# Performance work log

Hardware: AMD Instinct MI355X
Metric: run time of the kernel (lower is better)

Reference implementation:

```python
import jax, jax.numpy as jnp
import numpy as np

BETA = 0.25
GAMMA = 0.9
EPS = 1e-05
B, H, W, D, K = 64, 32, 32, 256, 1024


def setup_inputs() -> dict:
    key = jax.random.key(0)
    k1, k2 = jax.random.split(key)
    return {
        "inputs": jax.random.normal(k1, (B, H, W, D), dtype=jnp.float32),
        "codebook": jax.random.normal(k2, (D, K), dtype=jnp.float32),
        "ema_hidden_cluster": jnp.zeros((K,), dtype=jnp.float32),
        "ema_hidden_dw": jnp.zeros((D, K), dtype=jnp.float32),
        "counter": 1,  # counter after increment (fresh state: 0 + 1)
    }


def reference(inputs, codebook, ema_hidden_cluster, ema_hidden_dw, counter):
    d, k = codebook.shape
    flat = inputs.reshape(-1, d)  # [N, D]
    distances = (
        jnp.sum(jnp.square(flat), 1, keepdims=True)
        - 2.0 * jnp.matmul(flat, codebook)
        + jnp.sum(jnp.square(codebook), 0, keepdims=True)
    )
    encoding_indices = jnp.argmin(distances, axis=1)  # [N]
    encodings = jax.nn.one_hot(encoding_indices, k, dtype=distances.dtype)  # [N, K]
    flat_quantized = jnp.take(codebook, encoding_indices, axis=1).swapaxes(1, 0)  # [N, D]
    quantized = flat_quantized.reshape(inputs.shape)
    loss = BETA * jnp.mean(jnp.square(jax.lax.stop_gradient(quantized) - inputs))

    # --- EMA codebook update (training=True path) ---
    decay = jnp.float32(GAMMA)
    one = jnp.float32(1.0)
    bias = one - jnp.power(decay, counter)
    cluster_size = jnp.sum(encodings, axis=0)  # [K]
    hid_cs = ema_hidden_cluster * decay + cluster_size * (one - decay)
    avg_cs = hid_cs / bias
    dw = jnp.matmul(flat.T, encodings)  # [D, K]
    hid_dw = ema_hidden_dw * decay + dw * (one - decay)
    avg_dw = hid_dw / bias
    n = jnp.sum(avg_cs)
    smoothed_cs = (avg_cs + EPS) / (n + k * EPS) * n
    new_codebook = avg_dw / smoothed_cs[None, :]

    ste = inputs + jax.lax.stop_gradient(quantized - inputs)
    avg_probs = jnp.mean(encodings, 0)
    perplexity = jnp.exp(-jnp.sum(avg_probs * jnp.log(avg_probs + 1e-10)))
    return (ste, perplexity, loss, new_codebook)
```

## Files before the change

kernel.cpp:

```cpp
#include <hip/hip_runtime.h>

#define N 65536
#define D 256
#define K 1024
#define BETA 0.25f
#define GAMMA 0.9f
#define EPS 1e-5f

#define DWROWS 64

#define OFF_INDICES 0
#define OFF_PERM    262144
#define OFF_COUNTS  524288
#define OFF_CNORM   528384
#define OFF_OFFSETS 532480
#define OFF_CURSOR  536576
#define OFF_SMOOTH  540672
#define OFF_LOSSP   544768
#define OFF_CBT     546816
#define OFF_CBE     1595392

typedef __bf16 bf16x8 __attribute__((ext_vector_type(8)));
typedef short  s16x8  __attribute__((ext_vector_type(8)));
typedef float  f32x4  __attribute__((ext_vector_type(4)));

__device__ inline unsigned short f32_to_bf16_rn(float f) {
    unsigned int u = __float_as_uint(f);
    unsigned int r = u + 0x7fffu + ((u >> 16) & 1u);
    return (unsigned short)(r >> 16);
}

__device__ inline f32x4 mfma16(s16x8 a, s16x8 b, f32x4 c) {
    return __builtin_amdgcn_mfma_f32_16x16x32_bf16(
        __builtin_bit_cast(bf16x8, a), __builtin_bit_cast(bf16x8, b), c, 0, 0, 0);
}

__device__ __forceinline__ void stage16(const s16x8* __restrict__ g, s16x8* l) {
    __builtin_amdgcn_global_load_lds(
        (const __attribute__((address_space(1))) void*)g,
        (__attribute__((address_space(3))) void*)l, 16, 0, 0);
}

__global__ __launch_bounds__(256) void pack_cb(const float* __restrict__ cb,
                                               float* __restrict__ cbT,
                                               s16x8* __restrict__ cbEp,
                                               float* __restrict__ cnorm) {
    const int ct = blockIdx.x >> 2;
    const int c2 = blockIdx.x & 3;
#pragma unroll
    for (int it = 0; it < 2; ++it) {
        int u = it * 256 + threadIdx.x;
        int frgc = u >> 7;
        int ks = (u >> 6) & 1;
        int L = u & 63;
        int c = ct * 64 + frgc * 16 + (L & 15);
        int d0 = c2 * 64 + (ks * 4 + (L >> 4)) * 8;
        float v[8];
        s16x8 hv, lv;
        float ss = 0.f;
#pragma unroll
        for (int j = 0; j < 8; ++j) {
            float f = cb[(size_t)(d0 + j) * K + c];
            v[j] = f;
            unsigned short h = f32_to_bf16_rn(f);
            hv[j] = (short)h;
            lv[j] = (short)f32_to_bf16_rn(f - __uint_as_float((unsigned)h << 16));
            ss = fmaf(f, f, ss);
        }
        *(float4*)&cbT[(size_t)c * D + d0]     = make_float4(v[0], v[1], v[2], v[3]);
        *(float4*)&cbT[(size_t)c * D + d0 + 4] = make_float4(v[4], v[5], v[6], v[7]);
        cbEp[(size_t)(ct * 8 + c2) * 512 + u]     = hv;
        cbEp[(size_t)(ct * 8 + 4 + c2) * 512 + u] = lv;
        atomicAdd(&cnorm[c], ss);
    }
}

__global__ __launch_bounds__(256, 2) void argmin_mfma_kernel(
        const float* __restrict__ x,
        const s16x8* __restrict__ cbEp,
        const float* __restrict__ cnorm,
        int* __restrict__ indices) {
    __shared__ s16x8 Bs[2][1024];

    const int tid = threadIdx.x;
    const int lane = tid & 63;
    const int w = tid >> 6;
    const int r0 = blockIdx.x * 128;
    const int row16 = lane & 15;
    const int quad = lane >> 4;

#pragma unroll
    for (int i = 0; i < 4; ++i)
        stage16(cbEp + i * 256 + tid, &Bs[0][i * 256 + w * 64]);

    s16x8 Ah[2][8], Al[2][8];
#pragma unroll
    for (int frg = 0; frg < 2; ++frg) {
#pragma unroll
        for (int kb8 = 0; kb8 < 8; ++kb8) {
            const float* src = &x[(size_t)(r0 + w * 32 + frg * 16 + row16) * D
                                  + kb8 * 32 + quad * 8];
            float4 v0 = *(const float4*)src;
            float4 v1 = *(const float4*)(src + 4);
            float f[8] = {v0.x, v0.y, v0.z, v0.w, v1.x, v1.y, v1.z, v1.w};
            s16x8 hv, lv;
#pragma unroll
            for (int j = 0; j < 8; ++j) {
                unsigned short h = f32_to_bf16_rn(f[j]);
                hv[j] = (short)h;
                lv[j] = (short)f32_to_bf16_rn(f[j] - __uint_as_float((unsigned)h << 16));
            }
            Ah[frg][kb8] = hv;
            Al[frg][kb8] = lv;
        }
    }

    float minv[2][4];
    int   mini[2][4];
#pragma unroll
    for (int frg = 0; frg < 2; ++frg)
#pragma unroll
        for (int reg = 0; reg < 4; ++reg) { minv[frg][reg] = 3.4e38f; mini[frg][reg] = 0; }

    for (int ct = 0; ct < 16; ++ct) {
        f32x4 acc[2][4];
#pragma unroll
        for (int frg = 0; frg < 2; ++frg)
#pragma unroll
            for (int fc = 0; fc < 4; ++fc) acc[frg][fc] = (f32x4){0.f, 0.f, 0.f, 0.f};

#pragma unroll
        for (int ph = 0; ph < 4; ++ph) {
            __syncthreads();
            const bool has_next = !(ct == 15 && ph == 3);
            if (has_next) {
                const int nct = (ph == 3) ? ct + 1 : ct;
                const int nph = (ph == 3) ? 0 : ph + 1;
                const size_t gb = (size_t)(nct * 8 + nph * 2) * 512;
#pragma unroll
                for (int i = 0; i < 4; ++i)
                    stage16(cbEp + gb + i * 256 + tid, &Bs[(ph + 1) & 1][i * 256 + w * 64]);
            }
#pragma unroll
            for (int half = 0; half < 2; ++half) {
                const int cchunk = ph * 2 + half;
                const int c2 = cchunk & 3;
#pragma unroll
                for (int ks = 0; ks < 2; ++ks) {
                    const int ksb = c2 * 2 + ks;
#pragma unroll
                    for (int fc = 0; fc < 4; ++fc) {
                        s16x8 b = Bs[ph & 1][half * 512 + (fc * 2 + ks) * 64 + lane];
#pragma unroll
                        for (int frg = 0; frg < 2; ++frg) {
                            acc[frg][fc] = mfma16(Ah[frg][ksb], b, acc[frg][fc]);
                            if (cchunk < 4)
                                acc[frg][fc] = mfma16(Al[frg][ksb], b, acc[frg][fc]);
                        }
                    }
                }
            }
        }
#pragma unroll
        for (int fc = 0; fc < 4; ++fc) {
            int col = ct * 64 + fc * 16 + row16;
            float cn = cnorm[col];
#pragma unroll
            for (int frg = 0; frg < 2; ++frg)
#pragma unroll
                for (int reg = 0; reg < 4; ++reg) {
                    float val = fmaf(-2.f, acc[frg][fc][reg], cn);
                    if (val < minv[frg][reg]) { minv[frg][reg] = val; mini[frg][reg] = col; }
                }
        }
    }

#pragma unroll
    for (int mask = 1; mask <= 8; mask <<= 1) {
#pragma unroll
        for (int frg = 0; frg < 2; ++frg)
#pragma unroll
            for (int reg = 0; reg < 4; ++reg) {
                float ov = __shfl_xor(minv[frg][reg], mask, 64);
                int   oi = __shfl_xor(mini[frg][reg], mask, 64);
                if (ov < minv[frg][reg] ||
                    (ov == minv[frg][reg] && oi < mini[frg][reg])) {
                    minv[frg][reg] = ov; mini[frg][reg] = oi;
                }
            }
    }
    if (row16 == 0) {
#pragma unroll
        for (int frg = 0; frg < 2; ++frg)
#pragma unroll
            for (int reg = 0; reg < 4; ++reg)
                indices[r0 + w * 32 + frg * 16 + quad * 4 + reg] = mini[frg][reg];
    }
}

__global__ __launch_bounds__(1024) void finalize_kernel(const int* __restrict__ indices,
                                                        const float* __restrict__ ema_c,
                                                        const int* __restrict__ counter,
                                                        float* __restrict__ out_perp,
                                                        int* __restrict__ cursor,
                                                        float* __restrict__ smoothed) {
    const int k = threadIdx.x;
    __shared__ int hist[1024];
    __shared__ float fred[1024];
    __shared__ int scan[1024];
    __shared__ float nsum_s;

    hist[k] = 0;
    __syncthreads();
    const int4* idx4 = (const int4*)indices;
#pragma unroll 4
    for (int i = 0; i < 16; ++i) {
        int4 v = idx4[(size_t)i * 1024 + k];
        atomicAdd(&hist[v.x], 1);
        atomicAdd(&hist[v.y], 1);
        atomicAdd(&hist[v.z], 1);
        atomicAdd(&hist[v.w], 1);
    }
    __syncthreads();

    const int c = hist[k];
    const float bias = 1.0f - powf(GAMMA, (float)counter[0]);
    const float hid = fmaf(ema_c[k], GAMMA, (float)c * (1.0f - GAMMA));
    const float avg = hid / bias;

    fred[k] = avg;
    __syncthreads();
    for (int s = 512; s >= 1; s >>= 1) {
        if (k < s) fred[k] += fred[k + s];
        __syncthreads();
    }
    if (k == 0) nsum_s = fred[0];
    __syncthreads();
    const float nsum = nsum_s;

    float p = (float)c * (1.0f / (float)N);
    fred[k] = p * logf(p + 1e-10f);
    __syncthreads();
    for (int s = 512; s >= 1; s >>= 1) {
        if (k < s) fred[k] += fred[k + s];
        __syncthreads();
    }
    if (k == 0) out_perp[0] = expf(-fred[0]);

    scan[k] = c;
    __syncthreads();
    for (int s = 1; s < 1024; s <<= 1) {
        int v = (k >= s) ? scan[k - s] : 0;
        __syncthreads();
        scan[k] += v;
        __syncthreads();
    }
    cursor[k] = scan[k] - c;

    smoothed[k] = (avg + EPS) / (nsum + (float)K * EPS) * nsum;
}

__global__ __launch_bounds__(256) void scatter_kernel(const int* __restrict__ indices,
                                                      int* __restrict__ cursor,
                                                      int* __restrict__ permk,
                                                      float* __restrict__ dwT) {
    const int n = blockIdx.x * 256 + threadIdx.x;
    *(float4*)&dwT[(size_t)n * 4] = make_float4(0.f, 0.f, 0.f, 0.f);
    const int k = indices[n];
    const int pos = atomicAdd(&cursor[k], 1);
    permk[pos] = n | (k << 16);
}

__global__ __launch_bounds__(256) void dw_fused_kernel(const float* __restrict__ x,
                                                       const float* __restrict__ cbT,
                                                       const int* __restrict__ permk,
                                                       float* __restrict__ ste,
                                                       float* __restrict__ dwT,
                                                       float* __restrict__ lossp) {
    __shared__ int s_rows[DWROWS];
    __shared__ int s_keys[DWROWS + 1];
    const int d = threadIdx.x;
    const int base = blockIdx.x * DWROWS;
    if (threadIdx.x < DWROWS) {
        const int pk = permk[base + threadIdx.x];
        s_rows[threadIdx.x] = pk & 0xffff;
        s_keys[threadIdx.x] = pk >> 16;
    }
    if (threadIdx.x == 0) s_keys[DWROWS] = -1;
    __syncthreads();
    float acc = 0.f;
    float ls = 0.f;
#pragma unroll 4
    for (int i = 0; i < DWROWS; ++i) {
        const int n = s_rows[i];
        const int k = s_keys[i];
        const float xv = x[(size_t)n * D + d];
        const float q  = cbT[(size_t)k * D + d];
        ste[(size_t)n * D + d] = q;
        acc += xv;
        const float df = q - xv;
        ls = fmaf(df, df, ls);
        if (s_keys[i + 1] != k) {
            atomicAdd(&dwT[(size_t)k * D + d], acc);
            acc = 0.f;
        }
    }
#pragma unroll
    for (int off = 32; off >= 1; off >>= 1) ls += __shfl_down(ls, off, 64);
    __shared__ float red[4];
    if ((d & 63) == 0) red[d >> 6] = ls;
    __syncthreads();
    if (d == 0) lossp[blockIdx.x] = red[0] + red[1] + red[2] + red[3];
}

__global__ __launch_bounds__(256) void codebook_final_kernel(const float* __restrict__ dwT,
                                                             const float* __restrict__ ema_dw,
                                                             const float* __restrict__ smoothed,
                                                             const int* __restrict__ counter,
                                                             const float* __restrict__ lossp,
                                                             float* __restrict__ out_cb,
                                                             float* __restrict__ out_loss) {
    __shared__ float tile[64][65];
    __shared__ float lred[4];
    const int tid = threadIdx.x;

    if (blockIdx.x == 0) {
        float s = lossp[tid] + lossp[tid + 256] + lossp[tid + 512] + lossp[tid + 768];
#pragma unroll
        for (int off = 32; off >= 1; off >>= 1) s += __shfl_down(s, off, 64);
        if ((tid & 63) == 0) lred[tid >> 6] = s;
        __syncthreads();
        if (tid == 0)
            out_loss[0] = BETA * (lred[0] + lred[1] + lred[2] + lred[3])
                          * (1.0f / ((float)N * (float)D));
        __syncthreads();
    }

    const int d0 = (blockIdx.x & 3) * 64;
    const int k0 = (blockIdx.x >> 2) * 64;
#pragma unroll
    for (int it = 0; it < 16; ++it) {
        int idx = it * 256 + tid;
        int kk = idx >> 6, dd = idx & 63;
        tile[kk][dd] = dwT[(size_t)(k0 + kk) * D + d0 + dd];
    }
    __syncthreads();
    const float bias = 1.0f - powf(GAMMA, (float)counter[0]);
#pragma unroll
    for (int it = 0; it < 16; ++it) {
        int idx = it * 256 + tid;
        int dd = idx >> 6, kk = idx & 63;
        float dwv = tile[kk][dd];
        float hid = fmaf(ema_dw[(size_t)(d0 + dd) * K + k0 + kk], GAMMA,
                         dwv * (1.0f - GAMMA));
        out_cb[(size_t)(d0 + dd) * K + k0 + kk] = (hid / bias) / smoothed[k0 + kk];
    }
}

extern "C" void kernel_launch(void* const* d_in, const int* in_sizes, int n_in,
                              void* d_out, int out_size, void* d_ws, size_t ws_size,
                              hipStream_t stream) {
    const float* x       = (const float*)d_in[0];
    const float* cb      = (const float*)d_in[1];
    const float* ema_c   = (const float*)d_in[2];
    const float* ema_dw  = (const float*)d_in[3];
    const int*   counter = (const int*)d_in[4];

    float* out = (float*)d_out;
    float* ste = out;
    float* out_perp = out + (size_t)N * D;
    float* out_loss = out_perp + 1;
    float* out_cb = out_perp + 2;

    char* ws = (char*)d_ws;
    int* indices  = (int*)(ws + OFF_INDICES);
    int* permk    = (int*)(ws + OFF_PERM);
    float* cnorm  = (float*)(ws + OFF_CNORM);
    int* cursor   = (int*)(ws + OFF_CURSOR);
    float* smooth = (float*)(ws + OFF_SMOOTH);
    float* cbT    = (float*)(ws + OFF_CBT);
    s16x8* cbEp   = (s16x8*)(ws + OFF_CBE);
    float* dwT    = (float*)(ws + OFF_CBE);
    float* lossp  = (float*)(ws + OFF_CNORM);

    hipMemsetAsync(cnorm, 0, K * sizeof(float), stream);

    pack_cb<<<64, 256, 0, stream>>>(cb, cbT, cbEp, cnorm);
    argmin_mfma_kernel<<<N / 128, 256, 0, stream>>>(x, cbEp, cnorm, indices);
    finalize_kernel<<<1, 1024, 0, stream>>>(indices, ema_c, counter,
                                            out_perp, cursor, smooth);
    scatter_kernel<<<N / 256, 256, 0, stream>>>(indices, cursor, permk, dwT);
    dw_fused_kernel<<<N / DWROWS, 256, 0, stream>>>(x, cbT, permk, ste, dwT, lossp);
    codebook_final_kernel<<<64, 256, 0, stream>>>(dwT, ema_dw, smooth, counter,
                                                  lossp, out_cb, out_loss);
}
```

Baseline: 287.2 us.

## Vectorize dw gather, use wave shuffles in finalize, double pack_cb grid

Three separate changes. pack_cb now runs one item per thread across twice as many blocks. finalize_kernel replaces its shared-memory tree reductions and Hillis-Steele scan, with their many block barriers, by wave-level shuffle reductions and scans plus one barrier. dw_fused_kernel switches to float4 loads and stores, with each wave handling 16 rows, which cuts the load count but splits segment flushes per wave and adds four atomics per flush.

After: 308.6 us. 7.5% more time.

```diff
diff --git a/kernel.cpp b/kernel.cpp
--- a/kernel.cpp
+++ b/kernel.cpp
@@ -45,34 +45,32 @@
                                                float* __restrict__ cbT,
                                                s16x8* __restrict__ cbEp,
                                                float* __restrict__ cnorm) {
-    const int ct = blockIdx.x >> 2;
-    const int c2 = blockIdx.x & 3;
-#pragma unroll
-    for (int it = 0; it < 2; ++it) {
-        int u = it * 256 + threadIdx.x;
-        int frgc = u >> 7;
-        int ks = (u >> 6) & 1;
-        int L = u & 63;
-        int c = ct * 64 + frgc * 16 + (L & 15);
-        int d0 = c2 * 64 + (ks * 4 + (L >> 4)) * 8;
-        float v[8];
-        s16x8 hv, lv;
-        float ss = 0.f;
-#pragma unroll
-        for (int j = 0; j < 8; ++j) {
-            float f = cb[(size_t)(d0 + j) * K + c];
-            v[j] = f;
-            unsigned short h = f32_to_bf16_rn(f);
-            hv[j] = (short)h;
-            lv[j] = (short)f32_to_bf16_rn(f - __uint_as_float((unsigned)h << 16));
-            ss = fmaf(f, f, ss);
-        }
-        *(float4*)&cbT[(size_t)c * D + d0]     = make_float4(v[0], v[1], v[2], v[3]);
-        *(float4*)&cbT[(size_t)c * D + d0 + 4] = make_float4(v[4], v[5], v[6], v[7]);
-        cbEp[(size_t)(ct * 8 + c2) * 512 + u]     = hv;
-        cbEp[(size_t)(ct * 8 + 4 + c2) * 512 + u] = lv;
-        atomicAdd(&cnorm[c], ss);
-    }
+    const int ct = blockIdx.x >> 3;
+    const int c2 = (blockIdx.x >> 1) & 3;
+    const int half = blockIdx.x & 1;
+    const int u = half * 256 + threadIdx.x;
+    const int frgc = u >> 7;
+    const int ks = (u >> 6) & 1;
+    const int L = u & 63;
+    const int c = ct * 64 + frgc * 16 + (L & 15);
+    const int d0 = c2 * 64 + (ks * 4 + (L >> 4)) * 8;
+    float v[8];
+    s16x8 hv, lv;
+    float ss = 0.f;
+#pragma unroll
+    for (int j = 0; j < 8; ++j) {
+        float f = cb[(size_t)(d0 + j) * K + c];
+        v[j] = f;
+        unsigned short h = f32_to_bf16_rn(f);
+        hv[j] = (short)h;
+        lv[j] = (short)f32_to_bf16_rn(f - __uint_as_float((unsigned)h << 16));
+        ss = fmaf(f, f, ss);
+    }
+    *(float4*)&cbT[(size_t)c * D + d0]     = make_float4(v[0], v[1], v[2], v[3]);
+    *(float4*)&cbT[(size_t)c * D + d0 + 4] = make_float4(v[4], v[5], v[6], v[7]);
+    cbEp[(size_t)(ct * 8 + c2) * 512 + u]     = hv;
+    cbEp[(size_t)(ct * 8 + 4 + c2) * 512 + u] = lv;
+    atomicAdd(&cnorm[c], ss);
 }
 
 __global__ __launch_bounds__(256, 2) void argmin_mfma_kernel(
@@ -205,10 +203,11 @@
                                                         int* __restrict__ cursor,
                                                         float* __restrict__ smoothed) {
     const int k = threadIdx.x;
+    const int lane = k & 63;
+    const int wave = k >> 6;
     __shared__ int hist[1024];
-    __shared__ float fred[1024];
-    __shared__ int scan[1024];
-    __shared__ float nsum_s;
+    __shared__ float wsum[16], went[16];
+    __shared__ int wtot[16];
 
     hist[k] = 0;
     __syncthreads();
@@ -225,39 +224,37 @@
 
     const int c = hist[k];
     const float bias = 1.0f - powf(GAMMA, (float)counter[0]);
-    const float hid = fmaf(ema_c[k], GAMMA, (float)c * (1.0f - GAMMA));
-    const float avg = hid / bias;
-
-    fred[k] = avg;
-    __syncthreads();
-    for (int s = 512; s >= 1; s >>= 1) {
-        if (k < s) fred[k] += fred[k + s];
-        __syncthreads();
-    }
-    if (k == 0) nsum_s = fred[0];
-    __syncthreads();
-    const float nsum = nsum_s;
-
-    float p = (float)c * (1.0f / (float)N);
-    fred[k] = p * logf(p + 1e-10f);
-    __syncthreads();
-    for (int s = 512; s >= 1; s >>= 1) {
-        if (k < s) fred[k] += fred[k + s];
-        __syncthreads();
-    }
-    if (k == 0) out_perp[0] = expf(-fred[0]);
-
-    scan[k] = c;
-    __syncthreads();
-    for (int s = 1; s < 1024; s <<= 1) {
-        int v = (k >= s) ? scan[k - s] : 0;
-        __syncthreads();
-        scan[k] += v;
-        __syncthreads();
-    }
-    cursor[k] = scan[k] - c;
-
+    const float avg = fmaf(ema_c[k], GAMMA, (float)c * (1.0f - GAMMA)) / bias;
+    const float p = (float)c * (1.0f / (float)N);
+    const float ent = p * logf(p + 1e-10f);
+
+    float a = avg, e = ent;
+#pragma unroll
+    for (int off = 32; off >= 1; off >>= 1) {
+        a += __shfl_down(a, off, 64);
+        e += __shfl_down(e, off, 64);
+    }
+    int v = c;
+#pragma unroll
+    for (int off = 1; off < 64; off <<= 1) {
+        int t = __shfl_up(v, off, 64);
+        if (lane >= off) v += t;
+    }
+    if (lane == 0)  { wsum[wave] = a; went[wave] = e; }
+    if (lane == 63) { wtot[wave] = v; }
+    __syncthreads();
+
+    float nsum = 0.f, entt = 0.f;
+    int woff = 0;
+#pragma unroll
+    for (int i = 0; i < 16; ++i) {
+        nsum += wsum[i];
+        entt += went[i];
+        if (i < wave) woff += wtot[i];
+    }
+    cursor[k] = woff + v - c;
     smoothed[k] = (avg + EPS) / (nsum + (float)K * EPS) * nsum;
+    if (k == 0) out_perp[0] = expf(-entt);
 }
 
 __global__ __launch_bounds__(256) void scatter_kernel(const int* __restrict__ indices,
@@ -278,39 +275,53 @@
                                                        float* __restrict__ dwT,
                                                        float* __restrict__ lossp) {
     __shared__ int s_rows[DWROWS];
-    __shared__ int s_keys[DWROWS + 1];
-    const int d = threadIdx.x;
+    __shared__ int s_keys[DWROWS];
+    const int tid = threadIdx.x;
+    const int g = tid >> 6;
+    const int d4 = tid & 63;
     const int base = blockIdx.x * DWROWS;
-    if (threadIdx.x < DWROWS) {
-        const int pk = permk[base + threadIdx.x];
-        s_rows[threadIdx.x] = pk & 0xffff;
-        s_keys[threadIdx.x] = pk >> 16;
-    }
-    if (threadIdx.x == 0) s_keys[DWROWS] = -1;
-    __syncthreads();
-    float acc = 0.f;
+    if (tid < DWROWS) {
+        const int pk = permk[base + tid];
+        s_rows[tid] = pk & 0xffff;
+        s_keys[tid] = pk >> 16;
+    }
+    __syncthreads();
+
+    const float4* x4   = (const float4*)x;
+    const float4* cbT4 = (const float4*)cbT;
+    float4*       ste4 = (float4*)ste;
+
+    float ax = 0.f, ay = 0.f, az = 0.f, aw = 0.f;
     float ls = 0.f;
-#pragma unroll 4
-    for (int i = 0; i < DWROWS; ++i) {
-        const int n = s_rows[i];
-        const int k = s_keys[i];
-        const float xv = x[(size_t)n * D + d];
-        const float q  = cbT[(size_t)k * D + d];
-        ste[(size_t)n * D + d] = q;
-        acc += xv;
-        const float df = q - xv;
-        ls = fmaf(df, df, ls);
-        if (s_keys[i + 1] != k) {
-            atomicAdd(&dwT[(size_t)k * D + d], acc);
-            acc = 0.f;
+    const int r0 = g * 16;
+#pragma unroll
+    for (int i = 0; i < 16; ++i) {
+        const int r = r0 + i;
+        const int n = s_rows[r];
+        const int k = s_keys[r];
+        const float4 xv = x4[(size_t)n * 64 + d4];
+        const float4 q  = cbT4[(size_t)k * 64 + d4];
+        ste4[(size_t)n * 64 + d4] = q;
+        ax += xv.x; ay += xv.y; az += xv.z; aw += xv.w;
+        float dx = q.x - xv.x, dy = q.y - xv.y, dz = q.z - xv.z, dw = q.w - xv.w;
+        ls = fmaf(dx, dx, ls); ls = fmaf(dy, dy, ls);
+        ls = fmaf(dz, dz, ls); ls = fmaf(dw, dw, ls);
+        const int nk = (i == 15) ? -1 : s_keys[r + 1];
+        if (nk != k) {
+            float* dst = &dwT[(size_t)k * D + d4 * 4];
+            atomicAdd(dst + 0, ax);
+            atomicAdd(dst + 1, ay);
+            atomicAdd(dst + 2, az);
+            atomicAdd(dst + 3, aw);
+            ax = ay = az = aw = 0.f;
         }
     }
 #pragma unroll
     for (int off = 32; off >= 1; off >>= 1) ls += __shfl_down(ls, off, 64);
     __shared__ float red[4];
-    if ((d & 63) == 0) red[d >> 6] = ls;
-    __syncthreads();
-    if (d == 0) lossp[blockIdx.x] = red[0] + red[1] + red[2] + red[3];
+    if ((tid & 63) == 0) red[tid >> 6] = ls;
+    __syncthreads();
+    if (tid == 0) lossp[blockIdx.x] = red[0] + red[1] + red[2] + red[3];
 }
 
 __global__ __launch_bounds__(256) void codebook_final_kernel(const float* __restrict__ dwT,
@@ -385,7 +396,7 @@
 
     hipMemsetAsync(cnorm, 0, K * sizeof(float), stream);
 
-    pack_cb<<<64, 256, 0, stream>>>(cb, cbT, cbEp, cnorm);
+    pack_cb<<<128, 256, 0, stream>>>(cb, cbT, cbEp, cnorm);
     argmin_mfma_kernel<<<N / 128, 256, 0, stream>>>(x, cbEp, cnorm, indices);
     finalize_kernel<<<1, 1024, 0, stream>>>(indices, ema_c, counter,
                                             out_perp, cursor, smooth);
```
